# Performance work log

Measured on AMD Instinct MI355X. Metric: run time of the kernel, lower is better.

Reference implementation:

```python
import jax, jax.numpy as jnp
import numpy as np

B, D, H, L, T = 4096, 256, 512, 2, 45


def _lstm_cell(x, h, c, W_ih, W_hh, b_ih, b_hh):
    # PyTorch LSTM gate order: i, f, g, o
    gates = x @ W_ih + h @ W_hh + b_ih + b_hh  # [B, 4H]
    i, f, g, o = jnp.split(gates, 4, axis=-1)
    i = jax.nn.sigmoid(i)
    f = jax.nn.sigmoid(f)
    g = jnp.tanh(g)
    o = jax.nn.sigmoid(o)
    c_new = f * c + i * g
    h_new = o * jnp.tanh(c_new)
    return h_new, c_new


def setup_inputs() -> dict:
    key = jax.random.key(0)
    ks = jax.random.split(key, 32)
    s = 0.02
    inp = {
        "encoder_feat": jax.random.normal(ks[0], (B, D), jnp.float32),
        "context": jax.random.normal(ks[1], (B, D), jnp.float32),
        "initial_intent": jax.random.uniform(ks[2], (B, 1), jnp.float32),
        # hidden/cell init linears: d_model -> H*L (stored [in, out])
        "Wh_init": jax.random.normal(ks[3], (D, H * L), jnp.float32) * s,
        "bh_init": jnp.zeros((H * L,), jnp.float32),
        "Wc_init": jax.random.normal(ks[4], (D, H * L), jnp.float32) * s,
        "bc_init": jnp.zeros((H * L,), jnp.float32),
        # LSTM layer 0: input size 1 + d_model
        "W_ih0": jax.random.normal(ks[5], (1 + D, 4 * H), jnp.float32) * s,
        "W_hh0": jax.random.normal(ks[6], (H, 4 * H), jnp.float32) * s,
        "b_ih0": jnp.zeros((4 * H,), jnp.float32),
        "b_hh0": jnp.zeros((4 * H,), jnp.float32),
        # LSTM layer 1: input size H
        "W_ih1": jax.random.normal(ks[7], (H, 4 * H), jnp.float32) * s,
        "W_hh1": jax.random.normal(ks[8], (H, 4 * H), jnp.float32) * s,
        "b_ih1": jnp.zeros((4 * H,), jnp.float32),
        "b_hh1": jnp.zeros((4 * H,), jnp.float32),
        # output_proj: H -> 32 -> 1
        "Wo1": jax.random.normal(ks[9], (H, 32), jnp.float32) * s,
        "bo1": jnp.zeros((32,), jnp.float32),
        "Wo2": jax.random.normal(ks[10], (32, 1), jnp.float32) * s,
        "bo2": jnp.zeros((1,), jnp.float32),
        # global_intent_head: H -> 32 -> 1
        "Wg1": jax.random.normal(ks[11], (H, 32), jnp.float32) * s,
        "bg1": jnp.zeros((32,), jnp.float32),
        "Wg2": jax.random.normal(ks[12], (32, 1), jnp.float32) * s,
        "bg2": jnp.zeros((1,), jnp.float32),
    }
    return inp


def reference(encoder_feat, context, initial_intent,
              Wh_init, bh_init, Wc_init, bc_init,
              W_ih0, W_hh0, b_ih0, b_hh0,
              W_ih1, W_hh1, b_ih1, b_hh1,
              Wo1, bo1, Wo2, bo2, Wg1, bg1, Wg2, bg2):
    # init hidden/cell: [B, L*H] -> [B, L, H]; layer-major slices
    h_init = (encoder_feat @ Wh_init + bh_init).reshape(B, L, H)
    c_init = (encoder_feat @ Wc_init + bc_init).reshape(B, L, H)
    h0, h1 = h_init[:, 0], h_init[:, 1]
    c0, c1 = c_init[:, 0], c_init[:, 1]

    def step(carry, _):
        h0, c0, h1, c1, intent = carry
        x = jnp.concatenate([intent, context], axis=-1)  # [B, 1+D]
        h0n, c0n = _lstm_cell(x, h0, c0, W_ih0, W_hh0, b_ih0, b_hh0)
        h1n, c1n = _lstm_cell(h0n, h1, c1, W_ih1, W_hh1, b_ih1, b_hh1)
        logit = jax.nn.relu(h1n @ Wo1 + bo1) @ Wo2 + bo2  # [B, 1]
        intent_new = jax.nn.sigmoid(logit)
        return (h0n, c0n, h1n, c1n, intent_new), intent_new

    carry0 = (h0, c0, h1, c1, initial_intent)
    (h0, c0, h1, c1, _), ys = jax.lax.scan(step, carry0, None, length=T)
    step_intents = jnp.transpose(ys, (1, 0, 2))  # [B, T, 1]
    global_logit = jax.nn.relu(h1 @ Wg1 + bg1) @ Wg2 + bg2
    global_intent = jax.nn.sigmoid(global_logit)  # [B, 1]
    return step_intents, global_intent
```

## Files before the change

### kernel.cpp

```cpp
#include <hip/hip_runtime.h>
#include <hip/hip_bf16.h>

#define Bsz 4096
#define Dsz 256
#define Hsz 512
#define Tsz 45

typedef __attribute__((ext_vector_type(8))) short short8;
typedef __attribute__((ext_vector_type(4))) float f32x4;
typedef __attribute__((ext_vector_type(4))) unsigned short us4;
using bf16 = __hip_bfloat16;

__device__ __forceinline__ float sigf(float x)   { return 1.0f / (1.0f + __expf(-x)); }
__device__ __forceinline__ float tanhft(float x) { return 1.0f - 2.0f / (__expf(2.0f * x) + 1.0f); }
__device__ __forceinline__ float b2f(unsigned short u) { return __uint_as_float((unsigned)u << 16); }

__device__ __forceinline__ void gload16(const void* g, void* l) {
    __builtin_amdgcn_global_load_lds((const __attribute__((address_space(1))) void*)g,
                                     (__attribute__((address_space(3))) void*)l, 16, 0, 0);
}

__global__ void k_conv(const float* __restrict__ ef,   const float* __restrict__ ctx,
                       const float* __restrict__ Whi,  const float* __restrict__ Wci,
                       const float* __restrict__ Wih0, const float* __restrict__ Whh0,
                       const float* __restrict__ Wih1, const float* __restrict__ Whh1,
                       const float* __restrict__ Wo1,  const float* __restrict__ Wg1,
                       bf16* __restrict__ efb,  bf16* __restrict__ ctxb,
                       bf16* __restrict__ Wit,  bf16* __restrict__ Wt0,
                       bf16* __restrict__ Wt1,  bf16* __restrict__ Wo1t,
                       bf16* __restrict__ Wg1t)
{
    size_t tid = (size_t)blockIdx.x * blockDim.x + threadIdx.x;
    size_t gsz = (size_t)gridDim.x * blockDim.x;
    for (size_t i = tid; i < (size_t)Bsz * Dsz; i += gsz) {
        efb[i]  = __float2bfloat16(ef[i]);
        ctxb[i] = __float2bfloat16(ctx[i]);
    }
    for (size_t i = tid; i < 2048ull * 512; i += gsz) {
        size_t n = i >> 9, k = i & 511;
        Wt0[i] = __float2bfloat16(Whh0[k * 2048 + n]);
    }
    for (size_t i = tid; i < 2048ull * 1024; i += gsz) {
        size_t n = i >> 10, k = i & 1023;
        Wt1[i] = __float2bfloat16(k < 512 ? Wih1[k * 2048 + n] : Whh1[(k - 512) * 2048 + n]);
    }
    for (size_t i = tid; i < 32ull * 512; i += gsz) {
        size_t c = i >> 9, k = i & 511;
        Wo1t[i] = __float2bfloat16(Wo1[k * 32 + c]);
        Wg1t[i] = __float2bfloat16(Wg1[k * 32 + c]);
    }
    for (size_t i = tid; i < 4096ull * 256; i += gsz) {
        size_t n = i >> 8, k = i & 255;
        float v = (n < 1024) ? Whi[k * 1024 + n]
                : (n < 2048) ? Wci[k * 1024 + (n - 1024)]
                             : Wih0[(1 + k) * 2048 + (n - 2048)];
        Wit[i] = __float2bfloat16(v);
    }
}

__global__ void __launch_bounds__(256)
k_init(const bf16* __restrict__ efb, const bf16* __restrict__ ctxb,
       const bf16* __restrict__ Wit,
       const float* __restrict__ bh,  const float* __restrict__ bc,
       const float* __restrict__ bi0, const float* __restrict__ bh0,
       bf16* __restrict__ h0, bf16* __restrict__ h1,
       float* __restrict__ c0, float* __restrict__ c1,
       bf16* __restrict__ ctxg)
{
    const int t = threadIdx.x, lane = t & 63, w = t >> 6;
    const int wr = w >> 1, wc = w & 1;
    const int lq = lane >> 4, ln = lane & 15;
    const int m0 = blockIdx.x * 128, n0 = blockIdx.y * 64;
    const bf16* A = (n0 < 2048) ? efb : ctxb;

    f32x4 zero = {0.f, 0.f, 0.f, 0.f};
    f32x4 acc[4][2];
#pragma unroll
    for (int r = 0; r < 4; ++r)
#pragma unroll
        for (int c = 0; c < 2; ++c) acc[r][c] = zero;

    for (int k0 = 0; k0 < 256; k0 += 32) {
        short8 af[4];
#pragma unroll
        for (int r = 0; r < 4; ++r)
            af[r] = *(const short8*)(A + (size_t)(m0 + wr * 64 + r * 16 + ln) * 256 + k0 + lq * 8);
#pragma unroll
        for (int c = 0; c < 2; ++c) {
            short8 bv = *(const short8*)(Wit + (size_t)(n0 + wc * 32 + c * 16 + ln) * 256 + k0 + lq * 8);
#pragma unroll
            for (int r = 0; r < 4; ++r)
                acc[r][c] = __builtin_amdgcn_mfma_f32_16x16x32_bf16(af[r], bv, acc[r][c], 0, 0, 0);
        }
    }
#pragma unroll
    for (int r = 0; r < 4; ++r)
#pragma unroll
        for (int c = 0; c < 2; ++c)
#pragma unroll
            for (int e = 0; e < 4; ++e) {
                int b = m0 + wr * 64 + r * 16 + lq * 4 + e;
                int n = n0 + wc * 32 + c * 16 + ln;
                float v = acc[r][c][e];
                if (n < 1024) {
                    v += bh[n];
                    if (n < 512) h0[(size_t)b * 512 + n]       = __float2bfloat16(v);
                    else         h1[(size_t)b * 512 + n - 512] = __float2bfloat16(v);
                } else if (n < 2048) {
                    int m = n - 1024; v += bc[m];
                    if (m < 512) c0[(size_t)b * 512 + m]       = v;
                    else         c1[(size_t)b * 512 + m - 512] = v;
                } else {
                    int j = n - 2048;
                    ctxg[(size_t)b * 2048 + (j & 511) * 4 + (j >> 9)] =
                        __float2bfloat16(v + bi0[j] + bh0[j]);
                }
            }
}

__device__ __forceinline__ void intent_head(
    const bf16* __restrict__ h, const bf16* __restrict__ W1t,
    const float* __restrict__ b1, const float* __restrict__ W2, float b2s,
    int m0, float* sitp, float* outp, int ostride)
{
    const int t = threadIdx.x, lane = t & 63, w = t >> 6;
    const int lq = lane >> 4, ln = lane & 15;
    f32x4 zero = {0.f, 0.f, 0.f, 0.f};
    f32x4 acc[2][2];
#pragma unroll
    for (int r = 0; r < 2; ++r)
#pragma unroll
        for (int c = 0; c < 2; ++c) acc[r][c] = zero;

#pragma unroll
    for (int k0 = 0; k0 < 512; k0 += 32) {
        short8 av[2], bv[2];
#pragma unroll
        for (int r = 0; r < 2; ++r)
            av[r] = *(const short8*)(h + (size_t)(m0 + w * 32 + r * 16 + ln) * 512 + k0 + lq * 8);
#pragma unroll
        for (int c = 0; c < 2; ++c)
            bv[c] = *(const short8*)(W1t + (size_t)(c * 16 + ln) * 512 + k0 + lq * 8);
#pragma unroll
        for (int r = 0; r < 2; ++r)
#pragma unroll
            for (int c = 0; c < 2; ++c)
                acc[r][c] = __builtin_amdgcn_mfma_f32_16x16x32_bf16(av[r], bv[c], acc[r][c], 0, 0, 0);
    }
#pragma unroll
    for (int r = 0; r < 2; ++r)
#pragma unroll
        for (int e = 0; e < 4; ++e) {
            float v = 0.f;
#pragma unroll
            for (int c = 0; c < 2; ++c) {
                int col = c * 16 + ln;
                v += fmaxf(acc[r][c][e] + b1[col], 0.f) * W2[col];
            }
            v += __shfl_xor(v, 1);
            v += __shfl_xor(v, 2);
            v += __shfl_xor(v, 4);
            v += __shfl_xor(v, 8);
            int row = w * 32 + r * 16 + lq * 4 + e;
            if (ln == 0) {
                float p = sigf(v + b2s);
                if (sitp) sitp[row] = p;
                if (outp) outp[(size_t)(m0 + row) * ostride] = p;
            }
        }
}

template <int L0>
__device__ __forceinline__ void stage(const bf16* __restrict__ hA, const bf16* __restrict__ hB,
                                      const bf16* __restrict__ Wt,
                                      int m0, int j0, int k0, char* buf, int t)
{
    constexpr int KW = L0 ? 512 : 1024;
#pragma unroll
    for (int i = 0; i < 2; ++i) {
        int f = i * 256 + t;
        int row = f >> 2, slot = f & 3;
        int kk = k0 + ((slot ^ ((row >> 1) & 3)) << 3);
        const bf16* src;
        if (L0) src = hA + (size_t)(m0 + row) * Hsz + kk;
        else    src = (kk < 512) ? hA + (size_t)(m0 + row) * Hsz + kk
                                 : hB + (size_t)(m0 + row) * Hsz + (kk - 512);
        gload16(src, buf + (size_t)f * 16);
    }
#pragma unroll
    for (int i = 0; i < 2; ++i) {
        int f = i * 256 + t;
        int brow = f >> 2, slot = f & 3;
        int kc = slot ^ ((brow >> 1) & 3);
        gload16(Wt + (size_t)((brow >> 5) * 512 + j0 + (brow & 31)) * KW + k0 + kc * 8,
                buf + 8192 + (size_t)f * 16);
    }
}

__device__ __forceinline__ void mfma_tile(const char* buf,
                                          int wr, int wc, int lq, int ln,
                                          f32x4 (&acc)[4][4])
{
    const bf16* Ab = (const bf16*)buf;
    const bf16* Bb = (const bf16*)(buf + 8192);
    short8 af[4], bfr[4];
#pragma unroll
    for (int r = 0; r < 4; ++r) {
        int row = wr * 64 + r * 16 + ln;
        int slot = lq ^ ((row >> 1) & 3);
        af[r] = *(const short8*)(Ab + ((size_t)row * 4 + slot) * 8);
    }
#pragma unroll
    for (int g = 0; g < 4; ++g) {
        int brow = g * 32 + wc * 16 + ln;
        int slot = lq ^ ((brow >> 1) & 3);
        bfr[g] = *(const short8*)(Bb + ((size_t)brow * 4 + slot) * 8);
    }
#pragma unroll
    for (int g = 0; g < 4; ++g)
#pragma unroll
        for (int r = 0; r < 4; ++r)
            acc[g][r] = __builtin_amdgcn_mfma_f32_16x16x32_bf16(af[r], bfr[g], acc[g][r], 0, 0, 0);
}

#define WAIT_VM(N) asm volatile("s_waitcnt vmcnt(" #N ")" ::: "memory")

template <int L0>
__global__ void __launch_bounds__(256, 2)
k_gates(const bf16* __restrict__ hA, const bf16* __restrict__ hB,
        const bf16* __restrict__ Wt,
        const bf16* __restrict__ ctxg, const float* __restrict__ ii,
        const bf16* __restrict__ h1prev,
        const float* __restrict__ w0row,
        const float* __restrict__ b1, const float* __restrict__ b2,
        const bf16* __restrict__ Wo1t, const float* __restrict__ bo1,
        const float* __restrict__ Wo2, const float* __restrict__ bo2,
        float* __restrict__ cbuf, bf16* __restrict__ hout,
        float* __restrict__ outp, int step)
{
    constexpr int KW = L0 ? 512 : 1024;
    constexpr int NT = KW / 32;
    __shared__ __align__(16) char lds[65536];
    __shared__ float sitp[128];

    const int t = threadIdx.x, lane = t & 63, w = t >> 6;
    const int wr = w >> 1, wc = w & 1, lq = lane >> 4, ln = lane & 15;
    const int bid = blockIdx.x;
    const int xcd = bid & 7, idx = bid >> 3;
    const int mblk = xcd * 4 + (idx & 3), jblk = idx >> 2;
    const int j0 = jblk * 32, m0 = mblk * 128;

    stage<L0>(hA, hB, Wt, m0, j0, 0,  lds,         t);
    stage<L0>(hA, hB, Wt, m0, j0, 32, lds + 16384, t);
    stage<L0>(hA, hB, Wt, m0, j0, 64, lds + 32768, t);

    float sreg[16];
    if (L0) {
        if (step == 0) {
            if (t < 128) sitp[t] = ii[m0 + t];
        } else {
            intent_head(h1prev, Wo1t, bo1, Wo2, bo2[0], m0, sitp,
                        (jblk == 0) ? outp + (step - 1) : nullptr, Tsz);
        }
        asm volatile("s_waitcnt lgkmcnt(0)" ::: "memory");
        __builtin_amdgcn_s_barrier();
#pragma unroll
        for (int r = 0; r < 4; ++r)
#pragma unroll
            for (int e = 0; e < 4; ++e)
                sreg[r * 4 + e] = sitp[wr * 64 + r * 16 + lq * 4 + e];
    }

    f32x4 zero = {0.f, 0.f, 0.f, 0.f};
    f32x4 acc[4][4];
#pragma unroll
    for (int g = 0; g < 4; ++g)
#pragma unroll
        for (int r = 0; r < 4; ++r) acc[g][r] = zero;

#pragma unroll 4
    for (int kt = 0; kt < NT - 3; ++kt) {
        WAIT_VM(8);
        __builtin_amdgcn_s_barrier();
        mfma_tile(lds + (size_t)(kt & 3) * 16384, wr, wc, lq, ln, acc);
        stage<L0>(hA, hB, Wt, m0, j0, (kt + 3) * 32, lds + (size_t)((kt + 3) & 3) * 16384, t);
    }
    WAIT_VM(8);
    __builtin_amdgcn_s_barrier();
    mfma_tile(lds + (size_t)((NT - 3) & 3) * 16384, wr, wc, lq, ln, acc);
    WAIT_VM(4);
    __builtin_amdgcn_s_barrier();
    mfma_tile(lds + (size_t)((NT - 2) & 3) * 16384, wr, wc, lq, ln, acc);
    WAIT_VM(0);
    __builtin_amdgcn_s_barrier();
    mfma_tile(lds + (size_t)((NT - 1) & 3) * 16384, wr, wc, lq, ln, acc);

    const int jl = j0 + wc * 16 + ln;
    float addc[4];
#pragma unroll
    for (int g = 0; g < 4; ++g)
        addc[g] = L0 ? w0row[g * 512 + jl] : (b1[g * 512 + jl] + b2[g * 512 + jl]);

#pragma unroll
    for (int r = 0; r < 4; ++r)
#pragma unroll
        for (int e = 0; e < 4; ++e) {
            int b = m0 + wr * 64 + r * 16 + lq * 4 + e;
            float pre[4];
#pragma unroll
            for (int g = 0; g < 4; ++g) pre[g] = acc[g][r][e];
            if (L0) {
                float it = sreg[r * 4 + e];
                us4 cg = *(const us4*)((const unsigned short*)ctxg + (size_t)b * 2048 + jl * 4);
#pragma unroll
                for (int g = 0; g < 4; ++g) pre[g] += b2f(cg[g]) + it * addc[g];
            } else {
#pragma unroll
                for (int g = 0; g < 4; ++g) pre[g] += addc[g];
            }
            float ig = sigf(pre[0]), fg = sigf(pre[1]);
            float gg = tanhft(pre[2]), og = sigf(pre[3]);
            size_t idxb = (size_t)b * Hsz + jl;
            float cn = fg * cbuf[idxb] + ig * gg;
            cbuf[idxb] = cn;
            hout[idxb] = __float2bfloat16(og * tanhft(cn));
        }
}

__global__ void __launch_bounds__(256)
k_intent(const bf16* __restrict__ h, const bf16* __restrict__ W1t,
         const float* __restrict__ bias1, const float* __restrict__ W2,
         const float* __restrict__ bias2,
         float* __restrict__ outp, int ostride)
{
    intent_head(h, W1t, bias1, W2, bias2[0], blockIdx.x * 128, nullptr, outp, ostride);
}

extern "C" void kernel_launch(void* const* d_in, const int* in_sizes, int n_in,
                              void* d_out, int out_size, void* d_ws, size_t ws_size,
                              hipStream_t stream)
{
    const float* ef   = (const float*)d_in[0];
    const float* ctx  = (const float*)d_in[1];
    const float* ii   = (const float*)d_in[2];
    const float* Whi  = (const float*)d_in[3];
    const float* bh   = (const float*)d_in[4];
    const float* Wci  = (const float*)d_in[5];
    const float* bc   = (const float*)d_in[6];
    const float* Wih0 = (const float*)d_in[7];
    const float* Whh0 = (const float*)d_in[8];
    const float* bi0  = (const float*)d_in[9];
    const float* bh0  = (const float*)d_in[10];
    const float* Wih1 = (const float*)d_in[11];
    const float* Whh1 = (const float*)d_in[12];
    const float* bi1  = (const float*)d_in[13];
    const float* bh1  = (const float*)d_in[14];
    const float* Wo1  = (const float*)d_in[15];
    const float* bo1  = (const float*)d_in[16];
    const float* Wo2  = (const float*)d_in[17];
    const float* bo2  = (const float*)d_in[18];
    const float* Wg1  = (const float*)d_in[19];
    const float* bg1  = (const float*)d_in[20];
    const float* Wg2  = (const float*)d_in[21];
    const float* bg2  = (const float*)d_in[22];
    float* out = (float*)d_out;

    char* ws = (char*)d_ws;
    size_t off = 0;
    auto take = [&](size_t bytes) -> char* {
        char* pp = ws + off;
        off += (bytes + 255) & ~(size_t)255;
        return pp;
    };
    bf16* Wt0    = (bf16*)take(2048ull * 512 * 2);
    bf16* Wt1    = (bf16*)take(2048ull * 1024 * 2);
    bf16* Wo1t   = (bf16*)take(32ull * 512 * 2);
    bf16* Wg1t   = (bf16*)take(32ull * 512 * 2);
    bf16* Wit    = (bf16*)take(4096ull * 256 * 2);
    bf16* efb    = (bf16*)take((size_t)Bsz * Dsz * 2);
    bf16* ctxb   = (bf16*)take((size_t)Bsz * Dsz * 2);
    bf16* h0x    = (bf16*)take((size_t)Bsz * Hsz * 2);
    bf16* h0y    = (bf16*)take((size_t)Bsz * Hsz * 2);
    bf16* h1x    = (bf16*)take((size_t)Bsz * Hsz * 2);
    bf16* h1y    = (bf16*)take((size_t)Bsz * Hsz * 2);
    float* c0    = (float*)take((size_t)Bsz * Hsz * 4);
    float* c1    = (float*)take((size_t)Bsz * Hsz * 4);
    bf16* ctxg   = (bf16*)take((size_t)Bsz * 2048 * 2);
    (void)ws_size; (void)in_sizes; (void)n_in; (void)out_size;

    k_conv<<<2048, 256, 0, stream>>>(ef, ctx, Whi, Wci, Wih0, Whh0, Wih1, Whh1, Wo1, Wg1,
                                     efb, ctxb, Wit, Wt0, Wt1, Wo1t, Wg1t);
    k_init<<<dim3(32, 64), 256, 0, stream>>>(efb, ctxb, Wit, bh, bc, bi0, bh0,
                                             h0x, h1x, c0, c1, ctxg);

    for (int s = 0; s < Tsz; ++s) {
        int p = s & 1;
        const bf16* h0in  = p ? h0y : h0x;
        bf16*       h0out = p ? h0x : h0y;
        const bf16* h1in  = p ? h1y : h1x;
        bf16*       h1out = p ? h1x : h1y;
        k_gates<1><<<512, 256, 0, stream>>>(
            h0in, nullptr, Wt0, ctxg, ii, h1in, Wih0, nullptr, nullptr,
            Wo1t, bo1, Wo2, bo2, c0, h0out, out, s);
        k_gates<0><<<512, 256, 0, stream>>>(
            h0out, h1in, Wt1, nullptr, nullptr, nullptr, nullptr, bi1, bh1,
            nullptr, nullptr, nullptr, nullptr, c1, h1out, nullptr, s);
    }
    k_intent<<<32, 256, 0, stream>>>(h1y, Wo1t, bo1, Wo2, bo2, out + 44, Tsz);
    k_intent<<<32, 256, 0, stream>>>(h1y, Wg1t, bg1, Wg2, bg2, out + (size_t)Bsz * Tsz, 1);
}
```

Before: 2.724 ms.

## Enlarge gate GEMM tiles to 256x64 per block and split intent head into separate kernel

Each k_gates block now uses 512 threads and computes a 256-row by 64-column tile per gate (128 KB LDS, 4-stage buffer), which cuts the grid from 512 to 128 blocks and raises operand reuse per load. The per-step intent head is no longer recomputed redundantly inside every layer-0 block. It becomes its own k_intent launch after layer 1, which writes intents to a workspace read by the next step. The cost is one extra launch per step, only 128 blocks on a 256-CU device, and heavier register pressure from 32 accumulators per thread.

```diff
diff --git a/kernel.cpp b/kernel.cpp
--- a/kernel.cpp
+++ b/kernel.cpp
@@ -118,13 +118,15 @@
             }
 }
 
-__device__ __forceinline__ void intent_head(
-    const bf16* __restrict__ h, const bf16* __restrict__ W1t,
-    const float* __restrict__ b1, const float* __restrict__ W2, float b2s,
-    int m0, float* sitp, float* outp, int ostride)
+__global__ void __launch_bounds__(256)
+k_intent(const bf16* __restrict__ h, const bf16* __restrict__ W1t,
+         const float* __restrict__ bias1, const float* __restrict__ W2,
+         const float* __restrict__ bias2,
+         float* __restrict__ outp, int ostride, float* __restrict__ iws)
 {
     const int t = threadIdx.x, lane = t & 63, w = t >> 6;
     const int lq = lane >> 4, ln = lane & 15;
+    const int m0 = blockIdx.x * 128;
     f32x4 zero = {0.f, 0.f, 0.f, 0.f};
     f32x4 acc[2][2];
 #pragma unroll
@@ -155,7 +157,7 @@
 #pragma unroll
             for (int c = 0; c < 2; ++c) {
                 int col = c * 16 + ln;
-                v += fmaxf(acc[r][c][e] + b1[col], 0.f) * W2[col];
+                v += fmaxf(acc[r][c][e] + bias1[col], 0.f) * W2[col];
             }
             v += __shfl_xor(v, 1);
             v += __shfl_xor(v, 2);
@@ -163,9 +165,9 @@
             v += __shfl_xor(v, 8);
             int row = w * 32 + r * 16 + lq * 4 + e;
             if (ln == 0) {
-                float p = sigf(v + b2s);
-                if (sitp) sitp[row] = p;
-                if (outp) outp[(size_t)(m0 + row) * ostride] = p;
+                float p = sigf(v + bias2[0]);
+                outp[(size_t)(m0 + row) * ostride] = p;
+                if (iws) iws[m0 + row] = p;
             }
         }
 }
@@ -178,7 +180,7 @@
     constexpr int KW = L0 ? 512 : 1024;
 #pragma unroll
     for (int i = 0; i < 2; ++i) {
-        int f = i * 256 + t;
+        int f = i * 512 + t;
         int row = f >> 2, slot = f & 3;
         int kk = k0 + ((slot ^ ((row >> 1) & 3)) << 3);
         const bf16* src;
@@ -189,128 +191,106 @@
     }
 #pragma unroll
     for (int i = 0; i < 2; ++i) {
-        int f = i * 256 + t;
+        int f = i * 512 + t;
         int brow = f >> 2, slot = f & 3;
         int kc = slot ^ ((brow >> 1) & 3);
-        gload16(Wt + (size_t)((brow >> 5) * 512 + j0 + (brow & 31)) * KW + k0 + kc * 8,
-                buf + 8192 + (size_t)f * 16);
+        gload16(Wt + (size_t)((brow >> 6) * 512 + j0 + (brow & 63)) * KW + k0 + kc * 8,
+                buf + 16384 + (size_t)f * 16);
     }
 }
 
 __device__ __forceinline__ void mfma_tile(const char* buf,
-                                          int wr, int wc, int lq, int ln,
-                                          f32x4 (&acc)[4][4])
+                                          int wr, int wcg, int lq, int ln,
+                                          f32x4 (&acc)[4][8])
 {
     const bf16* Ab = (const bf16*)buf;
-    const bf16* Bb = (const bf16*)(buf + 8192);
-    short8 af[4], bfr[4];
-#pragma unroll
-    for (int r = 0; r < 4; ++r) {
-        int row = wr * 64 + r * 16 + ln;
+    const bf16* Bb = (const bf16*)(buf + 16384);
+    short8 af[8], bfr[4];
+#pragma unroll
+    for (int r = 0; r < 8; ++r) {
+        int row = wr * 128 + r * 16 + ln;
         int slot = lq ^ ((row >> 1) & 3);
         af[r] = *(const short8*)(Ab + ((size_t)row * 4 + slot) * 8);
     }
 #pragma unroll
     for (int g = 0; g < 4; ++g) {
-        int brow = g * 32 + wc * 16 + ln;
+        int brow = g * 64 + wcg * 16 + ln;
         int slot = lq ^ ((brow >> 1) & 3);
         bfr[g] = *(const short8*)(Bb + ((size_t)brow * 4 + slot) * 8);
     }
 #pragma unroll
     for (int g = 0; g < 4; ++g)
 #pragma unroll
-        for (int r = 0; r < 4; ++r)
+        for (int r = 0; r < 8; ++r)
             acc[g][r] = __builtin_amdgcn_mfma_f32_16x16x32_bf16(af[r], bfr[g], acc[g][r], 0, 0, 0);
 }
 
 #define WAIT_VM(N) asm volatile("s_waitcnt vmcnt(" #N ")" ::: "memory")
 
 template <int L0>
-__global__ void __launch_bounds__(256, 2)
+__global__ void __launch_bounds__(512)
 k_gates(const bf16* __restrict__ hA, const bf16* __restrict__ hB,
         const bf16* __restrict__ Wt,
-        const bf16* __restrict__ ctxg, const float* __restrict__ ii,
-        const bf16* __restrict__ h1prev,
+        const bf16* __restrict__ ctxg, const float* __restrict__ intent_src,
         const float* __restrict__ w0row,
         const float* __restrict__ b1, const float* __restrict__ b2,
-        const bf16* __restrict__ Wo1t, const float* __restrict__ bo1,
-        const float* __restrict__ Wo2, const float* __restrict__ bo2,
-        float* __restrict__ cbuf, bf16* __restrict__ hout,
-        float* __restrict__ outp, int step)
+        float* __restrict__ cbuf, bf16* __restrict__ hout)
 {
     constexpr int KW = L0 ? 512 : 1024;
     constexpr int NT = KW / 32;
-    __shared__ __align__(16) char lds[65536];
-    __shared__ float sitp[128];
+    __shared__ __align__(16) char lds[131072];
 
     const int t = threadIdx.x, lane = t & 63, w = t >> 6;
-    const int wr = w >> 1, wc = w & 1, lq = lane >> 4, ln = lane & 15;
+    const int wr = w >> 2, wcg = w & 3, lq = lane >> 4, ln = lane & 15;
     const int bid = blockIdx.x;
-    const int xcd = bid & 7, idx = bid >> 3;
-    const int mblk = xcd * 4 + (idx & 3), jblk = idx >> 2;
-    const int j0 = jblk * 32, m0 = mblk * 128;
-
-    stage<L0>(hA, hB, Wt, m0, j0, 0,  lds,         t);
-    stage<L0>(hA, hB, Wt, m0, j0, 32, lds + 16384, t);
-    stage<L0>(hA, hB, Wt, m0, j0, 64, lds + 32768, t);
-
-    float sreg[16];
-    if (L0) {
-        if (step == 0) {
-            if (t < 128) sitp[t] = ii[m0 + t];
-        } else {
-            intent_head(h1prev, Wo1t, bo1, Wo2, bo2[0], m0, sitp,
-                        (jblk == 0) ? outp + (step - 1) : nullptr, Tsz);
-        }
-        asm volatile("s_waitcnt lgkmcnt(0)" ::: "memory");
-        __builtin_amdgcn_s_barrier();
-#pragma unroll
-        for (int r = 0; r < 4; ++r)
-#pragma unroll
-            for (int e = 0; e < 4; ++e)
-                sreg[r * 4 + e] = sitp[wr * 64 + r * 16 + lq * 4 + e];
-    }
+    const int xcd = bid & 7, rem = bid >> 3;
+    const int mblk = xcd * 2 + (rem & 1), jblk = rem >> 1;
+    const int m0 = mblk * 256, j0 = jblk * 64;
+
+    stage<L0>(hA, hB, Wt, m0, j0, 0,  lds,          t);
+    stage<L0>(hA, hB, Wt, m0, j0, 32, lds + 32768,  t);
+    stage<L0>(hA, hB, Wt, m0, j0, 64, lds + 65536,  t);
 
     f32x4 zero = {0.f, 0.f, 0.f, 0.f};
-    f32x4 acc[4][4];
+    f32x4 acc[4][8];
 #pragma unroll
     for (int g = 0; g < 4; ++g)
 #pragma unroll
-        for (int r = 0; r < 4; ++r) acc[g][r] = zero;
+        for (int r = 0; r < 8; ++r) acc[g][r] = zero;
 
 #pragma unroll 4
     for (int kt = 0; kt < NT - 3; ++kt) {
         WAIT_VM(8);
         __builtin_amdgcn_s_barrier();
-        mfma_tile(lds + (size_t)(kt & 3) * 16384, wr, wc, lq, ln, acc);
-        stage<L0>(hA, hB, Wt, m0, j0, (kt + 3) * 32, lds + (size_t)((kt + 3) & 3) * 16384, t);
+        mfma_tile(lds + (size_t)(kt & 3) * 32768, wr, wcg, lq, ln, acc);
+        stage<L0>(hA, hB, Wt, m0, j0, (kt + 3) * 32, lds + (size_t)((kt + 3) & 3) * 32768, t);
     }
     WAIT_VM(8);
     __builtin_amdgcn_s_barrier();
-    mfma_tile(lds + (size_t)((NT - 3) & 3) * 16384, wr, wc, lq, ln, acc);
+    mfma_tile(lds + (size_t)((NT - 3) & 3) * 32768, wr, wcg, lq, ln, acc);
     WAIT_VM(4);
     __builtin_amdgcn_s_barrier();
-    mfma_tile(lds + (size_t)((NT - 2) & 3) * 16384, wr, wc, lq, ln, acc);
+    mfma_tile(lds + (size_t)((NT - 2) & 3) * 32768, wr, wcg, lq, ln, acc);
     WAIT_VM(0);
     __builtin_amdgcn_s_barrier();
-    mfma_tile(lds + (size_t)((NT - 1) & 3) * 16384, wr, wc, lq, ln, acc);
-
-    const int jl = j0 + wc * 16 + ln;
+    mfma_tile(lds + (size_t)((NT - 1) & 3) * 32768, wr, wcg, lq, ln, acc);
+
+    const int jl = j0 + wcg * 16 + ln;
     float addc[4];
 #pragma unroll
     for (int g = 0; g < 4; ++g)
         addc[g] = L0 ? w0row[g * 512 + jl] : (b1[g * 512 + jl] + b2[g * 512 + jl]);
 
 #pragma unroll
-    for (int r = 0; r < 4; ++r)
+    for (int r = 0; r < 8; ++r)
 #pragma unroll
         for (int e = 0; e < 4; ++e) {
-            int b = m0 + wr * 64 + r * 16 + lq * 4 + e;
+            int b = m0 + wr * 128 + r * 16 + lq * 4 + e;
             float pre[4];
 #pragma unroll
             for (int g = 0; g < 4; ++g) pre[g] = acc[g][r][e];
             if (L0) {
-                float it = sreg[r * 4 + e];
+                float it = intent_src[b];
                 us4 cg = *(const us4*)((const unsigned short*)ctxg + (size_t)b * 2048 + jl * 4);
 #pragma unroll
                 for (int g = 0; g < 4; ++g) pre[g] += b2f(cg[g]) + it * addc[g];
@@ -325,15 +305,6 @@
             cbuf[idxb] = cn;
             hout[idxb] = __float2bfloat16(og * tanhft(cn));
         }
-}
-
-__global__ void __launch_bounds__(256)
-k_intent(const bf16* __restrict__ h, const bf16* __restrict__ W1t,
-         const float* __restrict__ bias1, const float* __restrict__ W2,
-         const float* __restrict__ bias2,
-         float* __restrict__ outp, int ostride)
-{
-    intent_head(h, W1t, bias1, W2, bias2[0], blockIdx.x * 128, nullptr, outp, ostride);
 }
 
 extern "C" void kernel_launch(void* const* d_in, const int* in_sizes, int n_in,
@@ -386,6 +357,7 @@
     float* c0    = (float*)take((size_t)Bsz * Hsz * 4);
     float* c1    = (float*)take((size_t)Bsz * Hsz * 4);
     bf16* ctxg   = (bf16*)take((size_t)Bsz * 2048 * 2);
+    float* iws   = (float*)take((size_t)Bsz * 4);
     (void)ws_size; (void)in_sizes; (void)n_in; (void)out_size;
 
     k_conv<<<2048, 256, 0, stream>>>(ef, ctx, Whi, Wci, Wih0, Whh0, Wih1, Whh1, Wo1, Wg1,
@@ -399,13 +371,13 @@
         bf16*       h0out = p ? h0x : h0y;
         const bf16* h1in  = p ? h1y : h1x;
         bf16*       h1out = p ? h1x : h1y;
-        k_gates<1><<<512, 256, 0, stream>>>(
-            h0in, nullptr, Wt0, ctxg, ii, h1in, Wih0, nullptr, nullptr,
-            Wo1t, bo1, Wo2, bo2, c0, h0out, out, s);
-        k_gates<0><<<512, 256, 0, stream>>>(
-            h0out, h1in, Wt1, nullptr, nullptr, nullptr, nullptr, bi1, bh1,
-            nullptr, nullptr, nullptr, nullptr, c1, h1out, nullptr, s);
-    }
-    k_intent<<<32, 256, 0, stream>>>(h1y, Wo1t, bo1, Wo2, bo2, out + 44, Tsz);
-    k_intent<<<32, 256, 0, stream>>>(h1y, Wg1t, bg1, Wg2, bg2, out + (size_t)Bsz * Tsz, 1);
-}
+        const float* isrc = (s == 0) ? ii : iws;
+        k_gates<1><<<128, 512, 0, stream>>>(
+            h0in, nullptr, Wt0, ctxg, isrc, Wih0, nullptr, nullptr, c0, h0out);
+        k_gates<0><<<128, 512, 0, stream>>>(
+            h0out, h1in, Wt1, nullptr, nullptr, nullptr, bi1, bh1, c1, h1out);
+        k_intent<<<32, 256, 0, stream>>>(h1out, Wo1t, bo1, Wo2, bo2, out + s, Tsz, iws);
+    }
+    k_intent<<<32, 256, 0, stream>>>(h1y, Wg1t, bg1, Wg2, bg2,
+                                     out + (size_t)Bsz * Tsz, 1, nullptr);
+}
```

Result: slower. 4.061 ms (+49.1%).
